# Performance work log

Hardware: AMD Instinct MI355X
Metric: run time of the kernel (lower is better)

## Reference

```python
import jax, jax.numpy as jnp
import numpy as np

TEMPERATURE = 0.5


def setup_inputs() -> dict:
    key = jax.random.key(0)
    k1, k2 = jax.random.split(key)
    B, D = 4096, 256
    return {
        "features": jax.random.normal(k1, (B, D), dtype=jnp.float32),
        "transformed_features": jax.random.normal(k2, (B, D), dtype=jnp.float32),
    }


def reference(features, transformed_features):
    B = features.shape[0]
    N = 2 * B
    all_features = jnp.concatenate([features, transformed_features], axis=0)  # [2B, D]
    # F.normalize(dim=-1): L2 normalize with eps clamp of 1e-12 on the norm
    norm = jnp.maximum(jnp.linalg.norm(all_features, axis=-1, keepdims=True), 1e-12)
    all_features = all_features / norm
    sim = jnp.matmul(all_features, all_features.T)  # [2B, 2B]
    # positive pairs: diag at offsets +B and -B
    pos = jnp.concatenate([jnp.diagonal(sim, offset=B), jnp.diagonal(sim, offset=-B)], axis=0)  # [2B]
    numerator = jnp.exp(pos / TEMPERATURE)
    # torch code multiplies sim by (1 - eye) BEFORE exp, so diagonal contributes exp(0)=1 to the sum
    sim_no_diag = sim * (1.0 - jnp.eye(N, dtype=sim.dtype))
    denominator = jnp.exp(sim_no_diag / TEMPERATURE).sum(axis=1)  # [2B]
    losses = -jnp.log(numerator / denominator)
    return jnp.sum(losses) / N
```

## Files before the change

kernel.cpp:

```cpp
#include <hip/hip_runtime.h>

#define B_ROWS 4096
#define N_ROWS 8192
#define DDIM   256
#define IT2    2.885390081777927f

#define BM 128
#define BK 64
#define NTILE 64
#define NBLK  2080
#define NPARTS 128

typedef unsigned short ushort_t;
typedef __bf16 bf16x8 __attribute__((ext_vector_type(8)));
typedef float  f32x4  __attribute__((ext_vector_type(4)));

__device__ __forceinline__ ushort_t f2bf(float x) {
    union { float f; unsigned u; } a; a.f = x;
    unsigned r = a.u + 0x7fffu + ((a.u >> 16) & 1u);
    return (ushort_t)(r >> 16);
}

__device__ __forceinline__ void gload_lds16(const void* g, void* l) {
    __builtin_amdgcn_global_load_lds(
        (const __attribute__((address_space(1))) unsigned int*)g,
        (__attribute__((address_space(3))) unsigned int*)l,
        16, 0, 0);
}

__global__ __launch_bounds__(256) void k_norm_pos(
        const float* __restrict__ feats, const float* __restrict__ tfeats,
        ushort_t* __restrict__ Xb, float* __restrict__ posv) {
    __shared__ float fbuf[2][DDIM];
    __shared__ float nsh[4];
    int w = threadIdx.x >> 6, l = threadIdx.x & 63;
    int i0 = blockIdx.x * 2;
    int pair = (w < 2) ? w : (w - 2);
    int row  = (w < 2) ? (i0 + pair) : (i0 + pair + B_ROWS);
    const float* src = (w < 2) ? feats + (size_t)(i0 + pair) * DDIM
                               : tfeats + (size_t)(i0 + pair) * DDIM;
    float4 v = ((const float4*)src)[l];
    float ss = v.x*v.x + v.y*v.y + v.z*v.z + v.w*v.w;
    #pragma unroll
    for (int m = 1; m < 64; m <<= 1) ss += __shfl_xor(ss, m);
    float nrm = fmaxf(sqrtf(ss), 1e-12f);
    float inv = 1.0f / nrm;
    ushort4 o;
    o.x = f2bf(v.x * inv); o.y = f2bf(v.y * inv);
    o.z = f2bf(v.z * inv); o.w = f2bf(v.w * inv);
    ((ushort4*)(Xb + (size_t)row * DDIM))[l] = o;
    if (w < 2) ((float4*)fbuf[pair])[l] = v;
    if (l == 0) nsh[w] = nrm;
    __syncthreads();
    if (w >= 2) {
        float4 a = ((const float4*)fbuf[pair])[l];
        float d = a.x*v.x + a.y*v.y + a.z*v.z + a.w*v.w;
        #pragma unroll
        for (int m = 1; m < 64; m <<= 1) d += __shfl_xor(d, m);
        if (l == 0) posv[i0 + pair] = d / (nsh[pair] * nsh[w]);
    }
}

__global__ __launch_bounds__(256) void k_gemm(
        const ushort_t* __restrict__ Xb, float* __restrict__ parts) {
    __shared__ ushort_t ldsA[BM * BK];
    __shared__ ushort_t ldsB[BM * BK];

    int idx = blockIdx.x;
    int rt = 0;
    while (idx >= (NTILE - rt)) { idx -= (NTILE - rt); rt++; }
    int ct = rt + idx;
    bool isdiag = (rt == ct);

    int rowbase = rt * BM;
    int colbase = ct * BM;
    int t = threadIdx.x;
    int l = t & 63;
    int w = t >> 6;
    int wm = w >> 1, wn = w & 1;

    f32x4 acc[4][4];
    #pragma unroll
    for (int m = 0; m < 4; m++)
        #pragma unroll
        for (int n = 0; n < 4; n++) acc[m][n] = (f32x4){0.f, 0.f, 0.f, 0.f};

    for (int kb = 0; kb < DDIM; kb += BK) {
        #pragma unroll
        for (int i = 0; i < 4; i++) {
            int o   = (i * 256 + t) * 16;
            int row = o >> 7;
            int cb  = o & 127;
            int scb = cb ^ ((row & 7) << 4);
            const char* ga = (const char*)Xb +
                ((size_t)(rowbase + row) * DDIM + kb) * 2 + scb;
            gload_lds16(ga, (char*)ldsA + o);
            const char* gb = (const char*)Xb +
                ((size_t)(colbase + row) * DDIM + kb) * 2 + scb;
            gload_lds16(gb, (char*)ldsB + o);
        }
        __syncthreads();

        #pragma unroll
        for (int ks = 0; ks < 2; ks++) {
            bf16x8 af[4], bfr[4];
            int cbw = ((l >> 4) * 16) + ks * 64;
            #pragma unroll
            for (int m = 0; m < 4; m++) {
                int row  = wm * 64 + m * 16 + (l & 15);
                int addr = row * 128 + (cbw ^ ((row & 7) << 4));
                af[m] = *(const bf16x8*)((const char*)ldsA + addr);
            }
            #pragma unroll
            for (int n = 0; n < 4; n++) {
                int row  = wn * 64 + n * 16 + (l & 15);
                int addr = row * 128 + (cbw ^ ((row & 7) << 4));
                bfr[n] = *(const bf16x8*)((const char*)ldsB + addr);
            }
            #pragma unroll
            for (int m = 0; m < 4; m++)
                #pragma unroll
                for (int n = 0; n < 4; n++)
                    acc[m][n] = __builtin_amdgcn_mfma_f32_16x16x32_bf16(
                        af[m], bfr[n], acc[m][n], 0, 0, 0);
        }
        __syncthreads();
    }

    float rs[4][4];
    float cs[4];
    #pragma unroll
    for (int m = 0; m < 4; m++)
        #pragma unroll
        for (int j = 0; j < 4; j++) rs[m][j] = 0.0f;
    #pragma unroll
    for (int n = 0; n < 4; n++) cs[n] = 0.0f;

    #pragma unroll
    for (int m = 0; m < 4; m++) {
        #pragma unroll
        for (int j = 0; j < 4; j++) {
            int grow = rowbase + wm * 64 + m * 16 + (l >> 4) * 4 + j;
            #pragma unroll
            for (int n = 0; n < 4; n++) {
                int gcol = colbase + wn * 64 + n * 16 + (l & 15);
                float e = exp2f(acc[m][n][j] * IT2);
                if (isdiag && grow == gcol) e = 1.0f;
                rs[m][j] += e;
                cs[n]    += e;
            }
        }
    }

    #pragma unroll
    for (int m = 0; m < 4; m++)
        #pragma unroll
        for (int j = 0; j < 4; j++) {
            float v = rs[m][j];
            v += __shfl_xor(v, 1);
            v += __shfl_xor(v, 2);
            v += __shfl_xor(v, 4);
            v += __shfl_xor(v, 8);
            if ((l & 15) == 0) {
                int grow = rowbase + wm * 64 + m * 16 + (l >> 4) * 4 + j;
                parts[(size_t)(ct * 2 + wn) * N_ROWS + grow] = v;
            }
        }

    if (!isdiag) {
        #pragma unroll
        for (int n = 0; n < 4; n++) {
            float v = cs[n];
            v += __shfl_xor(v, 16);
            v += __shfl_xor(v, 32);
            if (l < 16) {
                int gcol = colbase + wn * 64 + n * 16 + l;
                parts[(size_t)(rt * 2 + wm) * N_ROWS + gcol] = v;
            }
        }
    }
}

__global__ __launch_bounds__(256) void k_rowreduce(
        const float* __restrict__ parts, float* __restrict__ bsums) {
    int row = blockIdx.x * 256 + threadIdx.x;
    float den = 0.0f;
    #pragma unroll 8
    for (int p = 0; p < NPARTS; p++) den += parts[(size_t)p * N_ROWS + row];
    float v = logf(den);
    #pragma unroll
    for (int m = 1; m < 64; m <<= 1) v += __shfl_xor(v, m);
    __shared__ float red[4];
    if ((threadIdx.x & 63) == 0) red[threadIdx.x >> 6] = v;
    __syncthreads();
    if (threadIdx.x == 0)
        bsums[blockIdx.x] = red[0] + red[1] + red[2] + red[3];
}

__global__ __launch_bounds__(256) void k_final(
        const float* __restrict__ bsums, const float* __restrict__ posv,
        float* __restrict__ out) {
    int t = threadIdx.x;
    float ps = 0.0f;
    for (int i = t; i < B_ROWS; i += 256) ps += posv[i];
    float lg = (t < 32) ? bsums[t] : 0.0f;
    float comb = lg - 4.0f * ps;
    #pragma unroll
    for (int m = 1; m < 64; m <<= 1) comb += __shfl_xor(comb, m);
    __shared__ float red[4];
    if ((t & 63) == 0) red[t >> 6] = comb;
    __syncthreads();
    if (t == 0) out[0] = (red[0] + red[1] + red[2] + red[3]) / (float)N_ROWS;
}

extern "C" void kernel_launch(void* const* d_in, const int* in_sizes, int n_in,
                              void* d_out, int out_size, void* d_ws, size_t ws_size,
                              hipStream_t stream) {
    const float* feats  = (const float*)d_in[0];
    const float* tfeats = (const float*)d_in[1];
    float* out = (float*)d_out;
    char* ws = (char*)d_ws;

    ushort_t* Xb    = (ushort_t*)ws;
    float*    posv  = (float*)(ws + 4194304);
    float*    parts = (float*)(ws + 4210688);
    float*    bsums = (float*)(ws + 8404992);

    k_norm_pos <<<B_ROWS / 2, 256, 0, stream>>>(feats, tfeats, Xb, posv);
    k_gemm     <<<NBLK, 256, 0, stream>>>(Xb, parts);
    k_rowreduce<<<N_ROWS / 256, 256, 0, stream>>>(parts, bsums);
    k_final    <<<1, 256, 0, stream>>>(bsums, posv, out);
}
```

Baseline: 115.9 us.

## Fuse all stages into one cooperative persistent kernel with row-chunked GEMM tiles

Merges normalization, positive-pair dot products, the symmetric GEMM with exp-sum, the row reduction and the final sum into one cooperative kernel separated by grid syncs, removing three extra launches. The GEMM now keeps a 128-row A tile in registers across chunks of up to five column tiles, loading full K=256 tiles into a single 64KB LDS buffer, which lowers the number of partial-sum slots. The costs are grid-wide barriers, fewer resident blocks from the larger LDS footprint, no overlap between loads and MFMA within a block, and a host-side occupancy query on every launch.

```diff
diff --git a/kernel.cpp b/kernel.cpp
--- a/kernel.cpp
+++ b/kernel.cpp
@@ -1,15 +1,18 @@
 #include <hip/hip_runtime.h>
+#include <hip/hip_cooperative_groups.h>
+
+namespace cg = cooperative_groups;
 
 #define B_ROWS 4096
 #define N_ROWS 8192
 #define DDIM   256
 #define IT2    2.885390081777927f
 
-#define BM 128
-#define BK 64
-#define NTILE 64
-#define NBLK  2080
-#define NPARTS 128
+#define NTILE  64
+#define CHUNK  5
+#define NCHUNK 442
+#define ROWSLOT0 64
+#define NPARTS 77
 
 typedef unsigned short ushort_t;
 typedef __bf16 bf16x8 __attribute__((ext_vector_type(8)));
@@ -28,189 +31,210 @@
         16, 0, 0);
 }
 
-__global__ __launch_bounds__(256) void k_norm_pos(
+__global__ __launch_bounds__(256, 2) void k_mega(
         const float* __restrict__ feats, const float* __restrict__ tfeats,
-        ushort_t* __restrict__ Xb, float* __restrict__ posv) {
-    __shared__ float fbuf[2][DDIM];
-    __shared__ float nsh[4];
-    int w = threadIdx.x >> 6, l = threadIdx.x & 63;
-    int i0 = blockIdx.x * 2;
-    int pair = (w < 2) ? w : (w - 2);
-    int row  = (w < 2) ? (i0 + pair) : (i0 + pair + B_ROWS);
-    const float* src = (w < 2) ? feats + (size_t)(i0 + pair) * DDIM
-                               : tfeats + (size_t)(i0 + pair) * DDIM;
-    float4 v = ((const float4*)src)[l];
-    float ss = v.x*v.x + v.y*v.y + v.z*v.z + v.w*v.w;
-    #pragma unroll
-    for (int m = 1; m < 64; m <<= 1) ss += __shfl_xor(ss, m);
-    float nrm = fmaxf(sqrtf(ss), 1e-12f);
-    float inv = 1.0f / nrm;
-    ushort4 o;
-    o.x = f2bf(v.x * inv); o.y = f2bf(v.y * inv);
-    o.z = f2bf(v.z * inv); o.w = f2bf(v.w * inv);
-    ((ushort4*)(Xb + (size_t)row * DDIM))[l] = o;
-    if (w < 2) ((float4*)fbuf[pair])[l] = v;
-    if (l == 0) nsh[w] = nrm;
-    __syncthreads();
-    if (w >= 2) {
-        float4 a = ((const float4*)fbuf[pair])[l];
-        float d = a.x*v.x + a.y*v.y + a.z*v.z + a.w*v.w;
-        #pragma unroll
-        for (int m = 1; m < 64; m <<= 1) d += __shfl_xor(d, m);
-        if (l == 0) posv[i0 + pair] = d / (nsh[pair] * nsh[w]);
-    }
-}
-
-__global__ __launch_bounds__(256) void k_gemm(
-        const ushort_t* __restrict__ Xb, float* __restrict__ parts) {
-    __shared__ ushort_t ldsA[BM * BK];
-    __shared__ ushort_t ldsB[BM * BK];
-
-    int idx = blockIdx.x;
-    int rt = 0;
-    while (idx >= (NTILE - rt)) { idx -= (NTILE - rt); rt++; }
-    int ct = rt + idx;
-    bool isdiag = (rt == ct);
-
-    int rowbase = rt * BM;
-    int colbase = ct * BM;
-    int t = threadIdx.x;
-    int l = t & 63;
-    int w = t >> 6;
-    int wm = w >> 1, wn = w & 1;
-
-    f32x4 acc[4][4];
-    #pragma unroll
-    for (int m = 0; m < 4; m++)
-        #pragma unroll
-        for (int n = 0; n < 4; n++) acc[m][n] = (f32x4){0.f, 0.f, 0.f, 0.f};
-
-    for (int kb = 0; kb < DDIM; kb += BK) {
-        #pragma unroll
-        for (int i = 0; i < 4; i++) {
-            int o   = (i * 256 + t) * 16;
-            int row = o >> 7;
-            int cb  = o & 127;
+        ushort_t* __restrict__ Xb, float* __restrict__ posv,
+        float* __restrict__ parts, float* __restrict__ bsums,
+        float* __restrict__ out) {
+    __shared__ ushort_t lds[128 * 256];
+    __shared__ float colred[4][128];
+    __shared__ float red[4];
+
+    cg::grid_group grid = cg::this_grid();
+    const int t = threadIdx.x, l = t & 63, w = t >> 6;
+    const int bid = blockIdx.x, nblk = gridDim.x;
+    const int nwav = nblk * 4, gw = bid * 4 + w;
+
+    for (int row = gw; row < N_ROWS; row += nwav) {
+        const float* src = (row < B_ROWS) ? feats + (size_t)row * DDIM
+                                          : tfeats + (size_t)(row - B_ROWS) * DDIM;
+        float4 v = ((const float4*)src)[l];
+        float ss = v.x*v.x + v.y*v.y + v.z*v.z + v.w*v.w;
+        #pragma unroll
+        for (int m = 1; m < 64; m <<= 1) ss += __shfl_xor(ss, m);
+        float inv = 1.0f / fmaxf(sqrtf(ss), 1e-12f);
+        ushort4 o;
+        o.x = f2bf(v.x * inv); o.y = f2bf(v.y * inv);
+        o.z = f2bf(v.z * inv); o.w = f2bf(v.w * inv);
+        ((ushort4*)(Xb + (size_t)row * DDIM))[l] = o;
+    }
+    for (int i = gw; i < B_ROWS; i += nwav) {
+        float4 a = ((const float4*)(feats  + (size_t)i * DDIM))[l];
+        float4 b = ((const float4*)(tfeats + (size_t)i * DDIM))[l];
+        float d  = a.x*b.x + a.y*b.y + a.z*b.z + a.w*b.w;
+        float sa = a.x*a.x + a.y*a.y + a.z*a.z + a.w*a.w;
+        float sb = b.x*b.x + b.y*b.y + b.z*b.z + b.w*b.w;
+        #pragma unroll
+        for (int m = 1; m < 64; m <<= 1) {
+            d += __shfl_xor(d, m); sa += __shfl_xor(sa, m); sb += __shfl_xor(sb, m);
+        }
+        if (l == 0) {
+            float na = fmaxf(sqrtf(sa), 1e-12f), nb = fmaxf(sqrtf(sb), 1e-12f);
+            posv[i] = d / (na * nb);
+        }
+    }
+    __threadfence();
+    grid.sync();
+
+    for (int c = bid; c < NCHUNK; c += nblk) {
+        int rem = c, rt = 0;
+        for (;;) {
+            int ncc = (NTILE - rt + CHUNK - 1) / CHUNK;
+            if (rem < ncc) break;
+            rem -= ncc; ++rt;
+        }
+        const int cc = rem;
+        const int rowbase = rt * 128;
+        const int ct0 = rt + cc * CHUNK;
+        int ctend = ct0 + CHUNK; if (ctend > NTILE) ctend = NTILE;
+
+        #pragma unroll
+        for (int i = 0; i < 16; i++) {
+            int o   = (t + i * 256) * 16;
+            int row = o >> 9, cb = o & 511;
             int scb = cb ^ ((row & 7) << 4);
-            const char* ga = (const char*)Xb +
-                ((size_t)(rowbase + row) * DDIM + kb) * 2 + scb;
-            gload_lds16(ga, (char*)ldsA + o);
-            const char* gb = (const char*)Xb +
-                ((size_t)(colbase + row) * DDIM + kb) * 2 + scb;
-            gload_lds16(gb, (char*)ldsB + o);
-        }
-        __syncthreads();
-
-        #pragma unroll
-        for (int ks = 0; ks < 2; ks++) {
-            bf16x8 af[4], bfr[4];
-            int cbw = ((l >> 4) * 16) + ks * 64;
-            #pragma unroll
-            for (int m = 0; m < 4; m++) {
-                int row  = wm * 64 + m * 16 + (l & 15);
-                int addr = row * 128 + (cbw ^ ((row & 7) << 4));
-                af[m] = *(const bf16x8*)((const char*)ldsA + addr);
-            }
-            #pragma unroll
-            for (int n = 0; n < 4; n++) {
-                int row  = wn * 64 + n * 16 + (l & 15);
-                int addr = row * 128 + (cbw ^ ((row & 7) << 4));
-                bfr[n] = *(const bf16x8*)((const char*)ldsB + addr);
-            }
-            #pragma unroll
-            for (int m = 0; m < 4; m++)
-                #pragma unroll
-                for (int n = 0; n < 4; n++)
-                    acc[m][n] = __builtin_amdgcn_mfma_f32_16x16x32_bf16(
-                        af[m], bfr[n], acc[m][n], 0, 0, 0);
-        }
-        __syncthreads();
-    }
-
-    float rs[4][4];
-    float cs[4];
-    #pragma unroll
-    for (int m = 0; m < 4; m++)
-        #pragma unroll
-        for (int j = 0; j < 4; j++) rs[m][j] = 0.0f;
-    #pragma unroll
-    for (int n = 0; n < 4; n++) cs[n] = 0.0f;
-
-    #pragma unroll
-    for (int m = 0; m < 4; m++) {
-        #pragma unroll
-        for (int j = 0; j < 4; j++) {
-            int grow = rowbase + wm * 64 + m * 16 + (l >> 4) * 4 + j;
-            #pragma unroll
-            for (int n = 0; n < 4; n++) {
-                int gcol = colbase + wn * 64 + n * 16 + (l & 15);
-                float e = exp2f(acc[m][n][j] * IT2);
-                if (isdiag && grow == gcol) e = 1.0f;
-                rs[m][j] += e;
-                cs[n]    += e;
-            }
-        }
-    }
-
-    #pragma unroll
-    for (int m = 0; m < 4; m++)
-        #pragma unroll
-        for (int j = 0; j < 4; j++) {
-            float v = rs[m][j];
-            v += __shfl_xor(v, 1);
-            v += __shfl_xor(v, 2);
-            v += __shfl_xor(v, 4);
-            v += __shfl_xor(v, 8);
-            if ((l & 15) == 0) {
-                int grow = rowbase + wm * 64 + m * 16 + (l >> 4) * 4 + j;
-                parts[(size_t)(ct * 2 + wn) * N_ROWS + grow] = v;
-            }
-        }
-
-    if (!isdiag) {
-        #pragma unroll
-        for (int n = 0; n < 4; n++) {
-            float v = cs[n];
-            v += __shfl_xor(v, 16);
-            v += __shfl_xor(v, 32);
-            if (l < 16) {
-                int gcol = colbase + wn * 64 + n * 16 + l;
-                parts[(size_t)(rt * 2 + wm) * N_ROWS + gcol] = v;
-            }
-        }
-    }
-}
-
-__global__ __launch_bounds__(256) void k_rowreduce(
-        const float* __restrict__ parts, float* __restrict__ bsums) {
-    int row = blockIdx.x * 256 + threadIdx.x;
-    float den = 0.0f;
-    #pragma unroll 8
-    for (int p = 0; p < NPARTS; p++) den += parts[(size_t)p * N_ROWS + row];
-    float v = logf(den);
-    #pragma unroll
-    for (int m = 1; m < 64; m <<= 1) v += __shfl_xor(v, m);
-    __shared__ float red[4];
-    if ((threadIdx.x & 63) == 0) red[threadIdx.x >> 6] = v;
-    __syncthreads();
-    if (threadIdx.x == 0)
-        bsums[blockIdx.x] = red[0] + red[1] + red[2] + red[3];
-}
-
-__global__ __launch_bounds__(256) void k_final(
-        const float* __restrict__ bsums, const float* __restrict__ posv,
-        float* __restrict__ out) {
-    int t = threadIdx.x;
-    float ps = 0.0f;
-    for (int i = t; i < B_ROWS; i += 256) ps += posv[i];
-    float lg = (t < 32) ? bsums[t] : 0.0f;
-    float comb = lg - 4.0f * ps;
-    #pragma unroll
-    for (int m = 1; m < 64; m <<= 1) comb += __shfl_xor(comb, m);
-    __shared__ float red[4];
-    if ((t & 63) == 0) red[t >> 6] = comb;
-    __syncthreads();
-    if (t == 0) out[0] = (red[0] + red[1] + red[2] + red[3]) / (float)N_ROWS;
+            gload_lds16((const char*)Xb + (size_t)(rowbase + row) * 512 + scb,
+                        (char*)lds + o);
+        }
+        __syncthreads();
+        bf16x8 af[2][8];
+        #pragma unroll
+        for (int m = 0; m < 2; m++) {
+            int rowA = w * 32 + m * 16 + (l & 15);
+            int sw = (rowA & 7) << 4;
+            #pragma unroll
+            for (int ks = 0; ks < 8; ks++) {
+                int cb = ks * 64 + ((l >> 4) << 4);
+                af[m][ks] = *(const bf16x8*)((const char*)lds + rowA * 512 + (cb ^ sw));
+            }
+        }
+        __syncthreads();
+
+        float rs[2][4] = {{0.f,0.f,0.f,0.f},{0.f,0.f,0.f,0.f}};
+
+        for (int ct = ct0; ct < ctend; ++ct) {
+            const int colbase = ct * 128;
+            const bool isdiag = (ct == rt);
+
+            #pragma unroll
+            for (int i = 0; i < 16; i++) {
+                int o   = (t + i * 256) * 16;
+                int row = o >> 9, cb = o & 511;
+                int scb = cb ^ ((row & 7) << 4);
+                gload_lds16((const char*)Xb + (size_t)(colbase + row) * 512 + scb,
+                            (char*)lds + o);
+            }
+            __syncthreads();
+
+            f32x4 acc[2][8];
+            #pragma unroll
+            for (int m = 0; m < 2; m++)
+                #pragma unroll
+                for (int n = 0; n < 8; n++) acc[m][n] = (f32x4){0.f,0.f,0.f,0.f};
+
+            #pragma unroll
+            for (int ks = 0; ks < 8; ks++) {
+                bf16x8 bfr[8];
+                int cb = ks * 64 + ((l >> 4) << 4);
+                #pragma unroll
+                for (int n = 0; n < 8; n++) {
+                    int rowB = n * 16 + (l & 15);
+                    bfr[n] = *(const bf16x8*)((const char*)lds +
+                                              rowB * 512 + (cb ^ ((rowB & 7) << 4)));
+                }
+                #pragma unroll
+                for (int m = 0; m < 2; m++)
+                    #pragma unroll
+                    for (int n = 0; n < 8; n++)
+                        acc[m][n] = __builtin_amdgcn_mfma_f32_16x16x32_bf16(
+                            af[m][ks], bfr[n], acc[m][n], 0, 0, 0);
+            }
+            __syncthreads();
+
+            float cs[8] = {0.f,0.f,0.f,0.f,0.f,0.f,0.f,0.f};
+            #pragma unroll
+            for (int m = 0; m < 2; m++) {
+                #pragma unroll
+                for (int j = 0; j < 4; j++) {
+                    int grow = rowbase + w * 32 + m * 16 + (l >> 4) * 4 + j;
+                    #pragma unroll
+                    for (int n = 0; n < 8; n++) {
+                        int gcol = colbase + n * 16 + (l & 15);
+                        float e = exp2f(acc[m][n][j] * IT2);
+                        if (isdiag && grow == gcol) e = 1.0f;
+                        rs[m][j] += e;
+                        cs[n]    += e;
+                    }
+                }
+            }
+
+            if (!isdiag) {
+                #pragma unroll
+                for (int n = 0; n < 8; n++) {
+                    float v = cs[n];
+                    v += __shfl_xor(v, 16);
+                    v += __shfl_xor(v, 32);
+                    if (l < 16) colred[w][n * 16 + l] = v;
+                }
+            }
+            __syncthreads();
+            if (!isdiag && t < 128) {
+                float s = colred[0][t] + colred[1][t] + colred[2][t] + colred[3][t];
+                parts[(size_t)rt * N_ROWS + colbase + t] = s;
+            }
+            __syncthreads();
+        }
+
+        #pragma unroll
+        for (int m = 0; m < 2; m++)
+            #pragma unroll
+            for (int j = 0; j < 4; j++) {
+                float v = rs[m][j];
+                v += __shfl_xor(v, 1); v += __shfl_xor(v, 2);
+                v += __shfl_xor(v, 4); v += __shfl_xor(v, 8);
+                if ((l & 15) == 0) {
+                    int grow = rowbase + w * 32 + m * 16 + (l >> 4) * 4 + j;
+                    parts[(size_t)(ROWSLOT0 + cc) * N_ROWS + grow] = v;
+                }
+            }
+    }
+    __threadfence();
+    grid.sync();
+
+    {
+        float lsum = 0.0f;
+        int tg = bid * 256 + t, nthr = nblk * 256;
+        for (int row = tg; row < N_ROWS; row += nthr) {
+            int rt = row >> 7;
+            int ncc = (NTILE - rt + CHUNK - 1) / CHUNK;
+            float den = 0.0f;
+            for (int s = 0; s < rt; s++)
+                den += parts[(size_t)s * N_ROWS + row];
+            for (int ccs = 0; ccs < ncc; ccs++)
+                den += parts[(size_t)(ROWSLOT0 + ccs) * N_ROWS + row];
+            lsum += logf(den);
+        }
+        float psum = 0.0f;
+        for (int i = tg; i < B_ROWS; i += nthr) psum += posv[i];
+        float comb = lsum - 4.0f * psum;
+        #pragma unroll
+        for (int m = 1; m < 64; m <<= 1) comb += __shfl_xor(comb, m);
+        if (l == 0) red[w] = comb;
+        __syncthreads();
+        if (t == 0) bsums[bid] = red[0] + red[1] + red[2] + red[3];
+    }
+    __threadfence();
+    grid.sync();
+
+    if (bid == 0) {
+        float v = 0.0f;
+        for (int i = t; i < nblk; i += 256) v += bsums[i];
+        #pragma unroll
+        for (int m = 1; m < 64; m <<= 1) v += __shfl_xor(v, m);
+        if (l == 0) red[w] = v;
+        __syncthreads();
+        if (t == 0) out[0] = (red[0] + red[1] + red[2] + red[3]) / (float)N_ROWS;
+    }
 }
 
 extern "C" void kernel_launch(void* const* d_in, const int* in_sizes, int n_in,
@@ -224,10 +248,16 @@
     ushort_t* Xb    = (ushort_t*)ws;
     float*    posv  = (float*)(ws + 4194304);
     float*    parts = (float*)(ws + 4210688);
-    float*    bsums = (float*)(ws + 8404992);
-
-    k_norm_pos <<<B_ROWS / 2, 256, 0, stream>>>(feats, tfeats, Xb, posv);
-    k_gemm     <<<NBLK, 256, 0, stream>>>(Xb, parts);
-    k_rowreduce<<<N_ROWS / 256, 256, 0, stream>>>(parts, bsums);
-    k_final    <<<1, 256, 0, stream>>>(bsums, posv, out);
-}
+    float*    bsums = (float*)(ws + 6733824);
+
+    int maxb = 0;
+    hipError_t e = hipOccupancyMaxActiveBlocksPerMultiprocessor(&maxb, k_mega, 256, 0);
+    if (e != hipSuccess || maxb < 1) maxb = 1;
+    int grid = maxb * 256;
+    if (grid > 2048) grid = 2048;
+
+    void* args[] = { (void*)&feats, (void*)&tfeats, (void*)&Xb, (void*)&posv,
+                     (void*)&parts, (void*)&bsums, (void*)&out };
+    hipLaunchCooperativeKernel((const void*)k_mega, dim3(grid), dim3(256),
+                               args, 0, stream);
+}
```

Measured after the change: 288.4 us. 149% more time.
